# Kernel tuning notes

Hardware: AMD Instinct MI355X
Metric: run time of the kernel (lower is better)

Reference implementation:

```python
import jax, jax.numpy as jnp
import numpy as np

E = 250000   # n_scanned_edges
B = 16       # batch_size
N = 50000    # n_entities (n_nodes)
R = 500      # n_relations
D_IN = 100   # input embedding dim (proj input)
D = 64       # n_dims_sm
M = 2 * E    # n_memorized_and_scanned_nodes (>= n_vi_groups + n_vj_groups)


def setup_inputs() -> dict:
    rng = np.random.default_rng(0)
    eg = rng.integers(0, B, E)
    vi = rng.integers(0, N, E)
    vj = rng.integers(0, N, E)
    order = np.lexsort((vj, vi, eg))  # sorted by (eg_idx, vi, vj) as the module assumes
    eg, vi, vj = eg[order], vi[order], vj[order]
    rel = rng.integers(0, R, E)
    # dense group ids; idx_vi is non-decreasing because edges are lexsorted by (eg,vi)
    idx_vi = np.unique(eg.astype(np.int64) * N + vi, return_inverse=True)[1]
    idx_vj = np.unique(eg.astype(np.int64) * N + vj, return_inverse=True)[1]
    n_vi = int(idx_vi.max()) + 1
    edges = np.stack([eg, vi, vj, rel, idx_vi, idx_vj, idx_vi, n_vi + idx_vj], 1).astype(np.int32)

    key = jax.random.key(0)
    ks = jax.random.split(key, 24)
    nrm = lambda k, shp, s=1.0: jax.random.normal(k, shp, jnp.float32) * s
    na = jax.random.uniform(ks[0], (B, N), jnp.float32)
    na = na / jnp.sum(na, 1, keepdims=True)  # node attention is a distribution per example
    inp = {
        "node_attention": na,
        "scanned_edges": jnp.asarray(edges),
        "hidden_uncon": nrm(ks[1], (1, N, D_IN)),
        "hidden_con": nrm(ks[2], (M, D_IN)),
        "rel_table": nrm(ks[3], (R, D_IN)),
        "query_head_emb": nrm(ks[4], (B, D_IN)),
        "query_rel_emb": nrm(ks[5], (B, D_IN)),
        "p_W": nrm(ks[6], (D_IN, D), 0.1),
        "p_b": jnp.zeros((D,), jnp.float32),
    }
    i = 7
    for g in ("g1", "g2"):
        for nm, shp in (("lW", (4 * D, D)), ("lb", (D,)), ("rW", (4 * D, D)), ("rb", (D,)), ("cW", (D, D)), ("cb", (D,))):
            inp[g + "_" + nm] = nrm(ks[i], shp, 0.05)
            i += 1
    return inp


def _g(left, right, lW, lb, rW, rb, cW, cb):
    # G layer: sum(left_dense(cat(left)) * center_dense(right_dense(cat(right))), -1)
    lx = jnp.concatenate(left, -1)
    rx = jnp.concatenate(right, -1)
    l = jax.nn.leaky_relu(lx @ lW + lb, 0.2)  # tf.nn.leaky_relu alpha=0.2
    r = jax.nn.leaky_relu(rx @ rW + rb, 0.2)
    return jnp.sum(l * (r @ cW + cb), -1)


def reference(node_attention, scanned_edges, hidden_uncon, hidden_con, rel_table,
              query_head_emb, query_rel_emb, p_W, p_b,
              g1_lW, g1_lb, g1_rW, g1_rb, g1_cW, g1_cb,
              g2_lW, g2_lb, g2_rW, g2_rb, g2_cW, g2_cb):
    Bn, Nn = node_attention.shape
    En = scanned_edges.shape[0]
    proj = lambda x: jnp.tanh(x @ p_W + p_b)

    h_con = proj(hidden_con)       # (M, D)
    h_uncon = proj(hidden_uncon)   # (1, N, D)
    qh = proj(query_head_emb)      # (B, D)
    qr = proj(query_rel_emb)

    e = scanned_edges
    eg, vi, vj = e[:, 0], e[:, 1], e[:, 2]
    idx_vi = e[:, 4]
    # node2edge gathers
    h_vi = h_con[e[:, 6]]          # (E, D)
    h_vj = h_con[e[:, 7]]
    hu_vj = h_uncon[0][vj]         # hidden_uncon batch is 1 -> idx 0
    remb = proj(rel_table[e[:, 3]])
    qhv = qh[eg]
    qrv = qr[eg]

    left = (h_vi, remb, qhv, qrv)
    logits = _g(left, (h_vj, remb, qhv, qrv), g1_lW, g1_lb, g1_rW, g1_rb, g1_cW, g1_cb)
    logits = logits + _g(left, (hu_vj, remb, qhv, qrv), g2_lW, g2_lb, g2_rW, g2_rb, g2_cW, g2_cb)

    # neighbor softmax over sorted idx_vi segments
    m = jax.ops.segment_max(logits, idx_vi, num_segments=En, indices_are_sorted=True)
    ex = jnp.exp(logits - m[idx_vi])
    den = jax.ops.segment_sum(ex, idx_vi, num_segments=En, indices_are_sorted=True)
    transition = ex / den[idx_vi]

    # flow attention: gather at (eg, vi), scatter-sum at (eg, vj)
    trans_att = node_attention[eg, vi] * transition
    new_att = jnp.zeros((Bn, Nn), node_attention.dtype).at[eg, vj].add(trans_att)
    new_att = new_att / jnp.sum(new_att, axis=1, keepdims=True)
    return new_att
```

## Files before the change

### kernel.cpp

```cpp
#include <hip/hip_runtime.h>

#define DIN 100
#define DD  64
#define NE  250000
#define NB  16
#define NN  50000
#define NR  500
#define NM  500000
#define NH  (NM + NN)

#define H_OFF    64
#define TA2_OFF  (H_OFF + NH*DD)
#define RT_OFF   (TA2_OFF + NE*DD)
#define QT_OFF   (RT_OFF + 4*NR*DD)
#define LG_OFF   (QT_OFF + 4*NB*DD)

#define PA 320
#define PB 160
#define PC 32

#define XT_STRIDE 260

__device__ __forceinline__ void fma4x4(const float4 x, const float4 w, float4 acc[4]) {
  acc[0].x += x.x*w.x; acc[0].y += x.x*w.y; acc[0].z += x.x*w.z; acc[0].w += x.x*w.w;
  acc[1].x += x.y*w.x; acc[1].y += x.y*w.y; acc[1].z += x.y*w.z; acc[1].w += x.y*w.w;
  acc[2].x += x.z*w.x; acc[2].y += x.z*w.y; acc[2].z += x.z*w.z; acc[2].w += x.z*w.w;
  acc[3].x += x.w*w.x; acc[3].y += x.w*w.y; acc[3].z += x.w*w.z; acc[3].w += x.w*w.w;
}

__device__ __forceinline__ float4 leaky4(float4 v) {
  v.x = v.x > 0.f ? v.x : 0.2f*v.x;
  v.y = v.y > 0.f ? v.y : 0.2f*v.y;
  v.z = v.z > 0.f ? v.z : 0.2f*v.z;
  v.w = v.w > 0.f ? v.w : 0.2f*v.w;
  return v;
}

__global__ void k_init(int* wsI, float* bsum) {
  if (threadIdx.x == 0) { wsI[0] = 0x7fffffff; wsI[1] = 0; }
  if (threadIdx.x < NB) bsum[threadIdx.x] = 0.f;
}

__global__ void k_limits(const int* __restrict__ edges, int* __restrict__ wsI) {
  int i = blockIdx.x * blockDim.x + threadIdx.x;
  int mn = 0x7fffffff, mx = -1;
  if (i < NE) { int v = edges[i*8 + 7]; mn = v; mx = v; }
  for (int off = 32; off > 0; off >>= 1) {
    mn = min(mn, __shfl_down(mn, off));
    mx = max(mx, __shfl_down(mx, off));
  }
  if ((threadIdx.x & 63) == 0) {
    atomicMin(&wsI[0], mn);
    atomicMax(&wsI[1], mx + 1);
  }
}

__global__ void k_tables(const float* __restrict__ rtab,
                         const float* __restrict__ qh, const float* __restrict__ qr,
                         const float* __restrict__ pW, const float* __restrict__ pb,
                         const float* __restrict__ g1_lW, const float* __restrict__ g1_lb,
                         const float* __restrict__ g1_rW, const float* __restrict__ g1_rb,
                         const float* __restrict__ g2_lW, const float* __restrict__ g2_lb,
                         const float* __restrict__ g2_rW, const float* __restrict__ g2_rb,
                         float* __restrict__ rT, float* __restrict__ qT) {
  __shared__ float xs[DIN], xs2[DIN], ps[DD], ps2[DD];
  const int d = threadIdx.x;
  const int blk = blockIdx.x;
  if (blk < NR) {
    for (int k = d; k < DIN; k += 64) xs[k] = rtab[blk*DIN + k];
    __syncthreads();
    float a = pb[d];
    for (int k = 0; k < DIN; ++k) a += xs[k] * pW[k*DD + d];
    ps[d] = tanhf(a);
    __syncthreads();
    float o1 = 0.f, o2 = 0.f, o3 = 0.f, o4 = 0.f;
    for (int k = 0; k < DD; ++k) {
      float p = ps[k];
      o1 += p * g1_lW[(DD + k)*DD + d];
      o2 += p * g1_rW[(DD + k)*DD + d];
      o3 += p * g2_lW[(DD + k)*DD + d];
      o4 += p * g2_rW[(DD + k)*DD + d];
    }
    rT[(0*NR + blk)*DD + d] = o1;
    rT[(1*NR + blk)*DD + d] = o2;
    rT[(2*NR + blk)*DD + d] = o3;
    rT[(3*NR + blk)*DD + d] = o4;
  } else {
    const int b = blk - NR;
    for (int k = d; k < DIN; k += 64) { xs[k] = qh[b*DIN + k]; xs2[k] = qr[b*DIN + k]; }
    __syncthreads();
    float a = pb[d], a2 = pb[d];
    for (int k = 0; k < DIN; ++k) { a += xs[k]*pW[k*DD + d]; a2 += xs2[k]*pW[k*DD + d]; }
    ps[d] = tanhf(a); ps2[d] = tanhf(a2);
    __syncthreads();
    float o1 = g1_lb[d], o2 = g1_rb[d], o3 = g2_lb[d], o4 = g2_rb[d];
    for (int k = 0; k < DD; ++k) {
      float p = ps[k], p2 = ps2[k];
      o1 += p * g1_lW[(2*DD + k)*DD + d] + p2 * g1_lW[(3*DD + k)*DD + d];
      o2 += p * g1_rW[(2*DD + k)*DD + d] + p2 * g1_rW[(3*DD + k)*DD + d];
      o3 += p * g2_lW[(2*DD + k)*DD + d] + p2 * g2_lW[(3*DD + k)*DD + d];
      o4 += p * g2_rW[(2*DD + k)*DD + d] + p2 * g2_rW[(3*DD + k)*DD + d];
    }
    qT[(0*NB + b)*DD + d] = o1;
    qT[(1*NB + b)*DD + d] = o2;
    qT[(2*NB + b)*DD + d] = o3;
    qT[(3*NB + b)*DD + d] = o4;
  }
}

__global__ __launch_bounds__(256, 2)
void k_proj(const float* __restrict__ hcon, const float* __restrict__ huncon,
            const float* __restrict__ pW, const float* __restrict__ pb,
            const int* __restrict__ lim, float* __restrict__ H) {
  __shared__ __align__(16) float pWs[DIN*DD];
  __shared__ __align__(16) float Xt[52][XT_STRIDE];
  const int tid = threadIdx.x;
  for (int i = tid; i < DIN*DD; i += 256) pWs[i] = pW[i];
  const int tc = tid & 7, tr = tid >> 3;
  const int c0 = tc << 3;
  const float4 pb0 = *(const float4*)&pb[c0];
  const float4 pb1 = *(const float4*)&pb[c0 + 4];
  const int nmax = lim[1];
  const int t_lo = (nmax + 255) >> 8;
  const int NT   = t_lo + ((NN + 255) >> 8);
  __syncthreads();
  for (int t = blockIdx.x; t < NT; t += gridDim.x) {
    const int row0 = (t < t_lo) ? (t << 8) : (NM + ((t - t_lo) << 8));
    const int myrow = row0 + tid;
    const float* src = nullptr;
    if (myrow < NH) src = (myrow < NM) ? &hcon[myrow*DIN] : &huncon[(myrow - NM)*DIN];
    float4 acc[2][2][4];
    #pragma unroll
    for (int a = 0; a < 2; ++a)
      #pragma unroll
      for (int b = 0; b < 2; ++b)
        #pragma unroll
        for (int i = 0; i < 4; ++i) acc[a][b][i] = make_float4(0.f,0.f,0.f,0.f);
    #pragma unroll
    for (int chunk = 0; chunk < 2; ++chunk) {
      const int kb = chunk ? 48 : 0;
      const int klen = chunk ? 52 : 48;
      __syncthreads();
      if (src) {
        for (int j = 0; j < klen; j += 4) {
          float4 v = *(const float4*)&src[kb + j];
          Xt[j+0][tid] = v.x; Xt[j+1][tid] = v.y; Xt[j+2][tid] = v.z; Xt[j+3][tid] = v.w;
        }
      }
      __syncthreads();
      for (int k = 0; k < klen; ++k) {
        float4 x0 = *(const float4*)&Xt[k][tr*8];
        float4 x1 = *(const float4*)&Xt[k][tr*8 + 4];
        float4 w0 = *(const float4*)&pWs[(kb + k)*DD + c0];
        float4 w1 = *(const float4*)&pWs[(kb + k)*DD + c0 + 4];
        fma4x4(x0, w0, acc[0][0]); fma4x4(x0, w1, acc[0][1]);
        fma4x4(x1, w0, acc[1][0]); fma4x4(x1, w1, acc[1][1]);
      }
    }
    #pragma unroll
    for (int a = 0; a < 2; ++a)
      #pragma unroll
      for (int i = 0; i < 4; ++i) {
        int row = row0 + tr*8 + a*4 + i;
        if (row < NH) {
          float4 o0, o1;
          o0.x = tanhf(acc[a][0][i].x + pb0.x);
          o0.y = tanhf(acc[a][0][i].y + pb0.y);
          o0.z = tanhf(acc[a][0][i].z + pb0.z);
          o0.w = tanhf(acc[a][0][i].w + pb0.w);
          o1.x = tanhf(acc[a][1][i].x + pb1.x);
          o1.y = tanhf(acc[a][1][i].y + pb1.y);
          o1.z = tanhf(acc[a][1][i].z + pb1.z);
          o1.w = tanhf(acc[a][1][i].w + pb1.w);
          *(float4*)&H[row*DD + c0]     = o0;
          *(float4*)&H[row*DD + c0 + 4] = o1;
        }
      }
  }
}

__global__ __launch_bounds__(256, 2)
void k_tf(const float* __restrict__ g1_lW, const float* __restrict__ g1_rW,
          const float* __restrict__ g2_lW, const float* __restrict__ g2_rW,
          const int* __restrict__ lim,
          float* __restrict__ H, float* __restrict__ TA2) {
  __shared__ __align__(16) float Ws0[DD*DD];
  __shared__ __align__(16) float Ws1[DD*DD];
  __shared__ __align__(16) float Ht[32][XT_STRIDE];
  const int tid = threadIdx.x;
  const int nvi  = lim[0];
  const int nmax = lim[1];
  int pool, pbase, pgrid;
  if (blockIdx.x < PA)           { pool = 0; pbase = blockIdx.x;           pgrid = PA; }
  else if (blockIdx.x < PA + PB) { pool = 1; pbase = blockIdx.x - PA;      pgrid = PB; }
  else                           { pool = 2; pbase = blockIdx.x - PA - PB; pgrid = PC; }
  if (pool == 0) {
    for (int i = tid; i < DD*DD; i += 256) { Ws0[i] = g1_lW[i]; Ws1[i] = g2_lW[i]; }
  } else if (pool == 1) {
    for (int i = tid; i < DD*DD; i += 256) Ws0[i] = g1_rW[i];
  } else {
    for (int i = tid; i < DD*DD; i += 256) Ws0[i] = g2_rW[i];
  }
  int t_begin, t_count, row_base;
  if (pool == 0)      { t_begin = 0;        t_count = (nvi + 255) >> 8;                 row_base = 0;  }
  else if (pool == 1) { t_begin = nvi >> 8; t_count = ((nmax + 255) >> 8) - (nvi >> 8); row_base = 0;  }
  else                { t_begin = 0;        t_count = (NN + 255) >> 8;                  row_base = NM; }
  const int tc = tid & 7, tr = tid >> 3;
  const int c0 = tc << 3;
  __syncthreads();
  for (int tt = pbase; tt < t_count; tt += pgrid) {
    const int row0 = row_base + ((t_begin + tt) << 8);
    const int myrow = row0 + tid;
    float4 a0[2][2][4], a1[2][2][4];
    #pragma unroll
    for (int a = 0; a < 2; ++a)
      #pragma unroll
      for (int b = 0; b < 2; ++b)
        #pragma unroll
        for (int i = 0; i < 4; ++i) {
          a0[a][b][i] = make_float4(0.f,0.f,0.f,0.f);
          a1[a][b][i] = make_float4(0.f,0.f,0.f,0.f);
        }
    #pragma unroll
    for (int chunk = 0; chunk < 2; ++chunk) {
      const int kb = chunk << 5;
      __syncthreads();
      if (myrow < NH) {
        const float* src = &H[myrow*DD + kb];
        #pragma unroll
        for (int j = 0; j < 32; j += 4) {
          float4 v = *(const float4*)&src[j];
          Ht[j+0][tid] = v.x; Ht[j+1][tid] = v.y; Ht[j+2][tid] = v.z; Ht[j+3][tid] = v.w;
        }
      }
      __syncthreads();
      if (pool == 0) {
        for (int k = 0; k < 32; ++k) {
          float4 x0 = *(const float4*)&Ht[k][tr*8];
          float4 x1 = *(const float4*)&Ht[k][tr*8 + 4];
          float4 w0 = *(const float4*)&Ws0[(kb + k)*DD + c0];
          float4 w1 = *(const float4*)&Ws0[(kb + k)*DD + c0 + 4];
          float4 u0 = *(const float4*)&Ws1[(kb + k)*DD + c0];
          float4 u1 = *(const float4*)&Ws1[(kb + k)*DD + c0 + 4];
          fma4x4(x0, w0, a0[0][0]); fma4x4(x0, w1, a0[0][1]);
          fma4x4(x1, w0, a0[1][0]); fma4x4(x1, w1, a0[1][1]);
          fma4x4(x0, u0, a1[0][0]); fma4x4(x0, u1, a1[0][1]);
          fma4x4(x1, u0, a1[1][0]); fma4x4(x1, u1, a1[1][1]);
        }
      } else {
        for (int k = 0; k < 32; ++k) {
          float4 x0 = *(const float4*)&Ht[k][tr*8];
          float4 x1 = *(const float4*)&Ht[k][tr*8 + 4];
          float4 w0 = *(const float4*)&Ws0[(kb + k)*DD + c0];
          float4 w1 = *(const float4*)&Ws0[(kb + k)*DD + c0 + 4];
          fma4x4(x0, w0, a0[0][0]); fma4x4(x0, w1, a0[0][1]);
          fma4x4(x1, w0, a0[1][0]); fma4x4(x1, w1, a0[1][1]);
        }
      }
    }
    #pragma unroll
    for (int a = 0; a < 2; ++a)
      #pragma unroll
      for (int i = 0; i < 4; ++i) {
        int row = row0 + tr*8 + a*4 + i;
        bool ok;
        if (pool == 0)      ok = (row < nvi);
        else if (pool == 1) ok = (row >= nvi && row < nmax);
        else                ok = (row < NH);
        if (ok) {
          *(float4*)&H[row*DD + c0]     = a0[a][0][i];
          *(float4*)&H[row*DD + c0 + 4] = a0[a][1][i];
          if (pool == 0) {
            *(float4*)&TA2[row*DD + c0]     = a1[a][0][i];
            *(float4*)&TA2[row*DD + c0 + 4] = a1[a][1][i];
          }
        }
      }
  }
}

__global__ __launch_bounds__(256, 2)
void k_edges(const int* __restrict__ edges,
             const float* __restrict__ TA, const float* __restrict__ TA2,
             const float* __restrict__ HU2,
             const float* __restrict__ rT, const float* __restrict__ qT,
             const float* __restrict__ cW1, const float* __restrict__ cb1,
             const float* __restrict__ cW2, const float* __restrict__ cb2,
             float* __restrict__ logits) {
  __shared__ __align__(16) float Wt1s[DD*68];
  __shared__ __align__(16) float Wt2s[DD*68];
  __shared__ __align__(16) float Lt[DD][68];
  __shared__ __align__(16) float Rt[DD][68];
  __shared__ __align__(16) float4 cbs4[2][16];
  __shared__ float lg[64];
  __shared__ int   se[64*8];
  const int tid = threadIdx.x;
  for (int i = tid; i < DD*DD; i += 256) {
    int k = i >> 6, d = i & 63;
    Wt1s[d*68 + k] = cW1[i];
    Wt2s[d*68 + k] = cW2[i];
  }
  if (tid < 16) {
    cbs4[0][tid] = *(const float4*)&cb1[tid*4];
    cbs4[1][tid] = *(const float4*)&cb2[tid*4];
  }
  const int e   = tid >> 2;
  const int d0  = (tid & 3) * 16;
  const int ee0 = (tid & 15) << 2;
  const int k0  = (tid >> 4) << 2;
  __syncthreads();
  const int NT = (NE + 63) / 64;
  for (int tile = blockIdx.x; tile < NT; tile += gridDim.x) {
    const int e0 = tile * 64;
    const int ecnt = min(64, NE - e0);
    for (int i = tid; i < 64*8; i += 256) se[i] = (i < ecnt*8) ? edges[e0*8 + i] : 0;
    if (tid < 64) lg[tid] = 0.f;
    __syncthreads();
    const int rel = se[e*8 + 3];
    const int eg  = se[e*8 + 0];
    const int li  = se[e*8 + 6];
    for (int g = 0; g < 2; ++g) {
      const float* Lb = g ? TA2 : TA;
      const float* Rb = g ? HU2 : TA;
      const float* rL = rT + (g ? 2*NR*DD : 0);
      const float* rR = rT + (g ? 3*NR*DD : 1*NR*DD);
      const float* qL = qT + (g ? 2*NB*DD : 0);
      const float* qR = qT + (g ? 3*NB*DD : 1*NB*DD);
      const float* Wts = g ? Wt2s : Wt1s;
      const int ri = g ? se[e*8 + 2] : se[e*8 + 7];
      float cbp = 0.f;
      #pragma unroll
      for (int di = 0; di < 4; ++di) {
        const int d = d0 + 4*di;
        float4 l = *(const float4*)&Lb[li*DD + d];
        float4 t = *(const float4*)&rL[rel*DD + d];
        float4 u = *(const float4*)&qL[eg*DD + d];
        l.x += t.x + u.x; l.y += t.y + u.y; l.z += t.z + u.z; l.w += t.w + u.w;
        l = leaky4(l);
        Lt[d+0][e] = l.x; Lt[d+1][e] = l.y; Lt[d+2][e] = l.z; Lt[d+3][e] = l.w;
        float4 c = cbs4[g][d >> 2];
        cbp += l.x*c.x + l.y*c.y + l.z*c.z + l.w*c.w;
        float4 r = *(const float4*)&Rb[ri*DD + d];
        t = *(const float4*)&rR[rel*DD + d];
        u = *(const float4*)&qR[eg*DD + d];
        r.x += t.x + u.x; r.y += t.y + u.y; r.z += t.z + u.z; r.w += t.w + u.w;
        r = leaky4(r);
        Rt[d+0][e] = r.x; Rt[d+1][e] = r.y; Rt[d+2][e] = r.z; Rt[d+3][e] = r.w;
      }
      atomicAdd(&lg[e], cbp);
      __syncthreads();
      float4 z[4] = {{0,0,0,0},{0,0,0,0},{0,0,0,0},{0,0,0,0}};
      for (int d = 0; d < DD; ++d) {
        float4 x = *(const float4*)&Lt[d][ee0];
        float4 w = *(const float4*)&Wts[d*68 + k0];
        fma4x4(x, w, z);
      }
      {
        float4 r0v = *(const float4*)&Rt[k0+0][ee0];
        float4 r1v = *(const float4*)&Rt[k0+1][ee0];
        float4 r2v = *(const float4*)&Rt[k0+2][ee0];
        float4 r3v = *(const float4*)&Rt[k0+3][ee0];
        float p0 = z[0].x*r0v.x + z[0].y*r1v.x + z[0].z*r2v.x + z[0].w*r3v.x;
        float p1 = z[1].x*r0v.y + z[1].y*r1v.y + z[1].z*r2v.y + z[1].w*r3v.y;
        float p2 = z[2].x*r0v.z + z[2].y*r1v.z + z[2].z*r2v.z + z[2].w*r3v.z;
        float p3 = z[3].x*r0v.w + z[3].y*r1v.w + z[3].z*r2v.w + z[3].w*r3v.w;
        atomicAdd(&lg[ee0+0], p0);
        atomicAdd(&lg[ee0+1], p1);
        atomicAdd(&lg[ee0+2], p2);
        atomicAdd(&lg[ee0+3], p3);
      }
      __syncthreads();
    }
    if (tid < ecnt) logits[e0 + tid] = lg[tid];
    __syncthreads();
  }
}

__global__ void k_softmax(const int* __restrict__ edges, const float* __restrict__ logits,
                          const float* __restrict__ na, float* __restrict__ out) {
  int e = blockIdx.x * blockDim.x + threadIdx.x;
  if (e >= NE) return;
  int seg = edges[e*8 + 4];
  if (e > 0 && edges[(e-1)*8 + 4] == seg) return;
  int j = e;
  float m = -1e30f;
  while (j < NE && edges[j*8 + 4] == seg) { m = fmaxf(m, logits[j]); ++j; }
  float s = 0.f;
  for (int t = e; t < j; ++t) s += expf(logits[t] - m);
  int eg = edges[e*8 + 0], vi = edges[e*8 + 1];
  float scale = na[eg*NN + vi] / s;
  for (int t = e; t < j; ++t) {
    int vj = edges[t*8 + 2];
    __hip_atomic_fetch_add(&out[eg*NN + vj], expf(logits[t] - m) * scale,
                           __ATOMIC_RELAXED, __HIP_MEMORY_SCOPE_AGENT);
  }
}

__global__ void k_rowsum(const float* __restrict__ out, float* __restrict__ bsum) {
  int b = blockIdx.y;
  float s = 0.f;
  for (int n = blockIdx.x * blockDim.x + threadIdx.x; n < NN; n += gridDim.x * blockDim.x)
    s += out[b*NN + n];
  for (int off = 32; off > 0; off >>= 1) s += __shfl_down(s, off);
  if ((threadIdx.x & 63) == 0)
    __hip_atomic_fetch_add(&bsum[b], s, __ATOMIC_RELAXED, __HIP_MEMORY_SCOPE_AGENT);
}

__global__ void k_div(float* __restrict__ out, const float* __restrict__ bsum) {
  int i = blockIdx.x * blockDim.x + threadIdx.x;
  if (i < NB*NN) out[i] /= bsum[i / NN];
}

extern "C" void kernel_launch(void* const* d_in, const int* in_sizes, int n_in,
                              void* d_out, int out_size, void* d_ws, size_t ws_size,
                              hipStream_t stream) {
  (void)in_sizes; (void)n_in; (void)out_size; (void)ws_size;
  const float* na     = (const float*)d_in[0];
  const int*   edges  = (const int*)  d_in[1];
  const float* huncon = (const float*)d_in[2];
  const float* hcon   = (const float*)d_in[3];
  const float* rtab   = (const float*)d_in[4];
  const float* qh     = (const float*)d_in[5];
  const float* qr     = (const float*)d_in[6];
  const float* pW     = (const float*)d_in[7];
  const float* pb     = (const float*)d_in[8];
  const float* g1_lW  = (const float*)d_in[9];
  const float* g1_lb  = (const float*)d_in[10];
  const float* g1_rW  = (const float*)d_in[11];
  const float* g1_rb  = (const float*)d_in[12];
  const float* g1_cW  = (const float*)d_in[13];
  const float* g1_cb  = (const float*)d_in[14];
  const float* g2_lW  = (const float*)d_in[15];
  const float* g2_lb  = (const float*)d_in[16];
  const float* g2_rW  = (const float*)d_in[17];
  const float* g2_rb  = (const float*)d_in[18];
  const float* g2_cW  = (const float*)d_in[19];
  const float* g2_cb  = (const float*)d_in[20];
  float* out  = (float*)d_out;
  float* ws   = (float*)d_ws;
  int*   wsI  = (int*)d_ws;
  float* bsum = ws + 16;
  float* H    = ws + H_OFF;
  float* TA2  = ws + TA2_OFF;
  float* rT   = ws + RT_OFF;
  float* qT   = ws + QT_OFF;
  float* lgp  = ws + LG_OFF;

  hipMemsetAsync(d_out, 0, (size_t)NB*NN*sizeof(float), stream);
  k_init<<<1, 64, 0, stream>>>(wsI, bsum);
  k_limits<<<(NE + 255)/256, 256, 0, stream>>>(edges, wsI);
  k_tables<<<NR + NB, 64, 0, stream>>>(rtab, qh, qr, pW, pb,
                                       g1_lW, g1_lb, g1_rW, g1_rb,
                                       g2_lW, g2_lb, g2_rW, g2_rb, rT, qT);
  k_proj<<<512, 256, 0, stream>>>(hcon, huncon, pW, pb, wsI, H);
  k_tf<<<PA + PB + PC, 256, 0, stream>>>(g1_lW, g1_rW, g2_lW, g2_rW, wsI, H, TA2);
  k_edges<<<512, 256, 0, stream>>>(edges, H, TA2, H + NM*DD, rT, qT,
                                   g1_cW, g1_cb, g2_cW, g2_cb, lgp);
  k_softmax<<<(NE + 255)/256, 256, 0, stream>>>(edges, lgp, na, out);
  k_rowsum<<<dim3(32, 16), 256, 0, stream>>>(out, bsum);
  k_div<<<(NB*NN + 255)/256, 256, 0, stream>>>(out, bsum);
}
```

Before: 813.7 us.

## Fuse projection and G-layer transforms into one per-row kernel with dynamic tiles

Replaces the separate projection kernel and the G-layer transform kernel with one fused kernel. Each thread now owns one row and computes the tanh projection in registers, stages it in shared memory, then applies the 64x64 transform weights read from global/scalar memory. This removes the H round-trip between the two passes. Work is handed out per wavefront of 64 rows through an atomic tile counter rather than fixed block pools. The cost is heavy register pressure from two 64-float arrays per thread and uncoalesced per-row input loads, with weights read from global memory instead of shared memory.

```diff
diff --git a/kernel.cpp b/kernel.cpp
--- a/kernel.cpp
+++ b/kernel.cpp
@@ -15,11 +15,8 @@
 #define QT_OFF   (RT_OFF + 4*NR*DD)
 #define LG_OFF   (QT_OFF + 4*NB*DD)
 
-#define PA 320
-#define PB 160
-#define PC 32
-
-#define XT_STRIDE 260
+#define GRID_PT  512
+#define NWAVES   (GRID_PT * 4)
 
 __device__ __forceinline__ void fma4x4(const float4 x, const float4 w, float4 acc[4]) {
   acc[0].x += x.x*w.x; acc[0].y += x.x*w.y; acc[0].z += x.x*w.z; acc[0].w += x.x*w.w;
@@ -37,7 +34,7 @@
 }
 
 __global__ void k_init(int* wsI, float* bsum) {
-  if (threadIdx.x == 0) { wsI[0] = 0x7fffffff; wsI[1] = 0; }
+  if (threadIdx.x == 0) { wsI[0] = 0x7fffffff; wsI[1] = 0; wsI[2] = NWAVES; }
   if (threadIdx.x < NB) bsum[threadIdx.x] = 0.f;
 }
 
@@ -108,174 +105,110 @@
   }
 }
 
+__device__ __forceinline__ void gemm64(const float* __restrict__ pcol,
+                                       const float* __restrict__ W,
+                                       float* __restrict__ o) {
+  #pragma unroll
+  for (int c = 0; c < DD; ++c) o[c] = 0.f;
+  float4 x4 = *(const float4*)pcol;
+  #pragma unroll 1
+  for (int kq = 0; kq < 16; ++kq) {
+    const float4 xc = x4;
+    if (kq + 1 < 16) x4 = *(const float4*)(pcol + 4*(kq+1));
+    const float* wk = W + kq*4*DD;
+    #pragma unroll
+    for (int c = 0; c < DD; ++c) o[c] += xc.x * wk[c];
+    #pragma unroll
+    for (int c = 0; c < DD; ++c) o[c] += xc.y * wk[DD + c];
+    #pragma unroll
+    for (int c = 0; c < DD; ++c) o[c] += xc.z * wk[2*DD + c];
+    #pragma unroll
+    for (int c = 0; c < DD; ++c) o[c] += xc.w * wk[3*DD + c];
+  }
+}
+
+__device__ __forceinline__ void store64(float* __restrict__ dst, const float* __restrict__ o) {
+  #pragma unroll
+  for (int q = 0; q < 16; ++q)
+    *(float4*)&dst[4*q] = make_float4(o[4*q], o[4*q+1], o[4*q+2], o[4*q+3]);
+}
+
 __global__ __launch_bounds__(256, 2)
-void k_proj(const float* __restrict__ hcon, const float* __restrict__ huncon,
-            const float* __restrict__ pW, const float* __restrict__ pb,
-            const int* __restrict__ lim, float* __restrict__ H) {
-  __shared__ __align__(16) float pWs[DIN*DD];
-  __shared__ __align__(16) float Xt[52][XT_STRIDE];
-  const int tid = threadIdx.x;
-  for (int i = tid; i < DIN*DD; i += 256) pWs[i] = pW[i];
-  const int tc = tid & 7, tr = tid >> 3;
-  const int c0 = tc << 3;
-  const float4 pb0 = *(const float4*)&pb[c0];
-  const float4 pb1 = *(const float4*)&pb[c0 + 4];
-  const int nmax = lim[1];
-  const int t_lo = (nmax + 255) >> 8;
-  const int NT   = t_lo + ((NN + 255) >> 8);
-  __syncthreads();
-  for (int t = blockIdx.x; t < NT; t += gridDim.x) {
-    const int row0 = (t < t_lo) ? (t << 8) : (NM + ((t - t_lo) << 8));
-    const int myrow = row0 + tid;
-    const float* src = nullptr;
-    if (myrow < NH) src = (myrow < NM) ? &hcon[myrow*DIN] : &huncon[(myrow - NM)*DIN];
-    float4 acc[2][2][4];
-    #pragma unroll
-    for (int a = 0; a < 2; ++a)
-      #pragma unroll
-      for (int b = 0; b < 2; ++b)
-        #pragma unroll
-        for (int i = 0; i < 4; ++i) acc[a][b][i] = make_float4(0.f,0.f,0.f,0.f);
-    #pragma unroll
-    for (int chunk = 0; chunk < 2; ++chunk) {
-      const int kb = chunk ? 48 : 0;
-      const int klen = chunk ? 52 : 48;
-      __syncthreads();
-      if (src) {
-        for (int j = 0; j < klen; j += 4) {
-          float4 v = *(const float4*)&src[kb + j];
-          Xt[j+0][tid] = v.x; Xt[j+1][tid] = v.y; Xt[j+2][tid] = v.z; Xt[j+3][tid] = v.w;
-        }
-      }
-      __syncthreads();
-      for (int k = 0; k < klen; ++k) {
-        float4 x0 = *(const float4*)&Xt[k][tr*8];
-        float4 x1 = *(const float4*)&Xt[k][tr*8 + 4];
-        float4 w0 = *(const float4*)&pWs[(kb + k)*DD + c0];
-        float4 w1 = *(const float4*)&pWs[(kb + k)*DD + c0 + 4];
-        fma4x4(x0, w0, acc[0][0]); fma4x4(x0, w1, acc[0][1]);
-        fma4x4(x1, w0, acc[1][0]); fma4x4(x1, w1, acc[1][1]);
-      }
-    }
-    #pragma unroll
-    for (int a = 0; a < 2; ++a)
-      #pragma unroll
-      for (int i = 0; i < 4; ++i) {
-        int row = row0 + tr*8 + a*4 + i;
-        if (row < NH) {
-          float4 o0, o1;
-          o0.x = tanhf(acc[a][0][i].x + pb0.x);
-          o0.y = tanhf(acc[a][0][i].y + pb0.y);
-          o0.z = tanhf(acc[a][0][i].z + pb0.z);
-          o0.w = tanhf(acc[a][0][i].w + pb0.w);
-          o1.x = tanhf(acc[a][1][i].x + pb1.x);
-          o1.y = tanhf(acc[a][1][i].y + pb1.y);
-          o1.z = tanhf(acc[a][1][i].z + pb1.z);
-          o1.w = tanhf(acc[a][1][i].w + pb1.w);
-          *(float4*)&H[row*DD + c0]     = o0;
-          *(float4*)&H[row*DD + c0 + 4] = o1;
-        }
-      }
-  }
-}
-
-__global__ __launch_bounds__(256, 2)
-void k_tf(const float* __restrict__ g1_lW, const float* __restrict__ g1_rW,
-          const float* __restrict__ g2_lW, const float* __restrict__ g2_rW,
-          const int* __restrict__ lim,
-          float* __restrict__ H, float* __restrict__ TA2) {
-  __shared__ __align__(16) float Ws0[DD*DD];
-  __shared__ __align__(16) float Ws1[DD*DD];
-  __shared__ __align__(16) float Ht[32][XT_STRIDE];
-  const int tid = threadIdx.x;
-  const int nvi  = lim[0];
-  const int nmax = lim[1];
-  int pool, pbase, pgrid;
-  if (blockIdx.x < PA)           { pool = 0; pbase = blockIdx.x;           pgrid = PA; }
-  else if (blockIdx.x < PA + PB) { pool = 1; pbase = blockIdx.x - PA;      pgrid = PB; }
-  else                           { pool = 2; pbase = blockIdx.x - PA - PB; pgrid = PC; }
-  if (pool == 0) {
-    for (int i = tid; i < DD*DD; i += 256) { Ws0[i] = g1_lW[i]; Ws1[i] = g2_lW[i]; }
-  } else if (pool == 1) {
-    for (int i = tid; i < DD*DD; i += 256) Ws0[i] = g1_rW[i];
-  } else {
-    for (int i = tid; i < DD*DD; i += 256) Ws0[i] = g2_rW[i];
-  }
-  int t_begin, t_count, row_base;
-  if (pool == 0)      { t_begin = 0;        t_count = (nvi + 255) >> 8;                 row_base = 0;  }
-  else if (pool == 1) { t_begin = nvi >> 8; t_count = ((nmax + 255) >> 8) - (nvi >> 8); row_base = 0;  }
-  else                { t_begin = 0;        t_count = (NN + 255) >> 8;                  row_base = NM; }
-  const int tc = tid & 7, tr = tid >> 3;
-  const int c0 = tc << 3;
-  __syncthreads();
-  for (int tt = pbase; tt < t_count; tt += pgrid) {
-    const int row0 = row_base + ((t_begin + tt) << 8);
-    const int myrow = row0 + tid;
-    float4 a0[2][2][4], a1[2][2][4];
-    #pragma unroll
-    for (int a = 0; a < 2; ++a)
-      #pragma unroll
-      for (int b = 0; b < 2; ++b)
-        #pragma unroll
-        for (int i = 0; i < 4; ++i) {
-          a0[a][b][i] = make_float4(0.f,0.f,0.f,0.f);
-          a1[a][b][i] = make_float4(0.f,0.f,0.f,0.f);
-        }
-    #pragma unroll
-    for (int chunk = 0; chunk < 2; ++chunk) {
-      const int kb = chunk << 5;
-      __syncthreads();
-      if (myrow < NH) {
-        const float* src = &H[myrow*DD + kb];
-        #pragma unroll
-        for (int j = 0; j < 32; j += 4) {
-          float4 v = *(const float4*)&src[j];
-          Ht[j+0][tid] = v.x; Ht[j+1][tid] = v.y; Ht[j+2][tid] = v.z; Ht[j+3][tid] = v.w;
-        }
-      }
-      __syncthreads();
-      if (pool == 0) {
-        for (int k = 0; k < 32; ++k) {
-          float4 x0 = *(const float4*)&Ht[k][tr*8];
-          float4 x1 = *(const float4*)&Ht[k][tr*8 + 4];
-          float4 w0 = *(const float4*)&Ws0[(kb + k)*DD + c0];
-          float4 w1 = *(const float4*)&Ws0[(kb + k)*DD + c0 + 4];
-          float4 u0 = *(const float4*)&Ws1[(kb + k)*DD + c0];
-          float4 u1 = *(const float4*)&Ws1[(kb + k)*DD + c0 + 4];
-          fma4x4(x0, w0, a0[0][0]); fma4x4(x0, w1, a0[0][1]);
-          fma4x4(x1, w0, a0[1][0]); fma4x4(x1, w1, a0[1][1]);
-          fma4x4(x0, u0, a1[0][0]); fma4x4(x0, u1, a1[0][1]);
-          fma4x4(x1, u0, a1[1][0]); fma4x4(x1, u1, a1[1][1]);
-        }
-      } else {
-        for (int k = 0; k < 32; ++k) {
-          float4 x0 = *(const float4*)&Ht[k][tr*8];
-          float4 x1 = *(const float4*)&Ht[k][tr*8 + 4];
-          float4 w0 = *(const float4*)&Ws0[(kb + k)*DD + c0];
-          float4 w1 = *(const float4*)&Ws0[(kb + k)*DD + c0 + 4];
-          fma4x4(x0, w0, a0[0][0]); fma4x4(x0, w1, a0[0][1]);
-          fma4x4(x1, w0, a0[1][0]); fma4x4(x1, w1, a0[1][1]);
-        }
-      }
-    }
-    #pragma unroll
-    for (int a = 0; a < 2; ++a)
-      #pragma unroll
-      for (int i = 0; i < 4; ++i) {
-        int row = row0 + tr*8 + a*4 + i;
-        bool ok;
-        if (pool == 0)      ok = (row < nvi);
-        else if (pool == 1) ok = (row >= nvi && row < nmax);
-        else                ok = (row < NH);
-        if (ok) {
-          *(float4*)&H[row*DD + c0]     = a0[a][0][i];
-          *(float4*)&H[row*DD + c0 + 4] = a0[a][1][i];
-          if (pool == 0) {
-            *(float4*)&TA2[row*DD + c0]     = a1[a][0][i];
-            *(float4*)&TA2[row*DD + c0 + 4] = a1[a][1][i];
-          }
-        }
-      }
+void k_projtf(const float* __restrict__ hcon, const float* __restrict__ huncon,
+              const float* __restrict__ pW, const float* __restrict__ pb,
+              const float* __restrict__ g1_lW, const float* __restrict__ g1_rW,
+              const float* __restrict__ g2_lW, const float* __restrict__ g2_rW,
+              int* __restrict__ wsI,
+              float* __restrict__ H, float* __restrict__ TA2) {
+  __shared__ __align__(16) float Pb[256][68];
+  const int tid  = threadIdx.x;
+  const int lane = tid & 63;
+  const int nvi  = wsI[0];
+  const int nmax = wsI[1];
+  const int T0  = (nvi + 63) >> 6;
+  const int T1b = nvi >> 6;
+  const int T1  = ((nmax + 63) >> 6) - T1b;
+  const int T2  = (NN + 63) >> 6;
+  const int total = T0 + T1 + T2;
+  float* pcol = &Pb[tid][0];
+
+  int t = (int)blockIdx.x * 4 + (tid >> 6);
+  for (;;) {
+    if (t >= total) break;
+    int pool, row0;
+    if (t < T0)           { pool = 0; row0 = t << 6; }
+    else if (t < T0 + T1) { pool = 1; row0 = (T1b + (t - T0)) << 6; }
+    else                  { pool = 2; row0 = NM + ((t - T0 - T1) << 6); }
+    const int row = row0 + lane;
+    int rrow = row;
+    if (pool == 2) { if (rrow >= NH) rrow = NH - 1; }
+    else           { if (rrow >= NM) rrow = NM - 1; }
+    const float4* src4 = (const float4*)((pool == 2)
+        ? (huncon + (size_t)(rrow - NM) * DIN)
+        : (hcon   + (size_t)rrow * DIN));
+
+    float p[DD];
+    #pragma unroll
+    for (int c = 0; c < DD; ++c) p[c] = 0.f;
+    float4 v = src4[0];
+    #pragma unroll 1
+    for (int j = 0; j < 25; ++j) {
+      const float4 vc = v;
+      if (j + 1 < 25) v = src4[j + 1];
+      const float* wj = pW + j * 4 * DD;
+      #pragma unroll
+      for (int c = 0; c < DD; ++c) p[c] += vc.x * wj[c];
+      #pragma unroll
+      for (int c = 0; c < DD; ++c) p[c] += vc.y * wj[DD + c];
+      #pragma unroll
+      for (int c = 0; c < DD; ++c) p[c] += vc.z * wj[2*DD + c];
+      #pragma unroll
+      for (int c = 0; c < DD; ++c) p[c] += vc.w * wj[3*DD + c];
+    }
+    #pragma unroll
+    for (int c = 0; c < DD; ++c) p[c] = tanhf(p[c] + pb[c]);
+
+    #pragma unroll
+    for (int q = 0; q < 16; ++q)
+      *(float4*)(pcol + 4*q) = make_float4(p[4*q], p[4*q+1], p[4*q+2], p[4*q+3]);
+
+    float o[DD];
+    if (pool == 0) {
+      gemm64(pcol, g1_lW, o);
+      if (row < nvi) store64(&H[(size_t)row*DD], o);
+      gemm64(pcol, g2_lW, o);
+      if (row < nvi) store64(&TA2[(size_t)row*DD], o);
+    } else if (pool == 1) {
+      gemm64(pcol, g1_rW, o);
+      if (row >= nvi && row < nmax) store64(&H[(size_t)row*DD], o);
+    } else {
+      gemm64(pcol, g2_rW, o);
+      if (row < NH) store64(&H[(size_t)row*DD], o);
+    }
+
+    int nt = 0;
+    if (lane == 0) nt = atomicAdd(&wsI[2], 1);
+    t = __shfl(nt, 0);
   }
 }
 
@@ -452,8 +385,8 @@
   k_tables<<<NR + NB, 64, 0, stream>>>(rtab, qh, qr, pW, pb,
                                        g1_lW, g1_lb, g1_rW, g1_rb,
                                        g2_lW, g2_lb, g2_rW, g2_rb, rT, qT);
-  k_proj<<<512, 256, 0, stream>>>(hcon, huncon, pW, pb, wsI, H);
-  k_tf<<<PA + PB + PC, 256, 0, stream>>>(g1_lW, g1_rW, g2_lW, g2_rW, wsI, H, TA2);
+  k_projtf<<<GRID_PT, 256, 0, stream>>>(hcon, huncon, pW, pb,
+                                        g1_lW, g1_rW, g2_lW, g2_rW, wsI, H, TA2);
   k_edges<<<512, 256, 0, stream>>>(edges, H, TA2, H + NM*DD, rT, qT,
                                    g1_cW, g1_cb, g2_cW, g2_cb, lgp);
   k_softmax<<<(NE + 255)/256, 256, 0, stream>>>(edges, lgp, na, out);
```

New measurement: 925.0 us. 1.14x slower.
